# Kernel optimization log

Hardware: AMD Instinct MI355X
Metric: run time of the kernel (lower is better)

Reference implementation:

```python
import jax, jax.numpy as jnp
import numpy as np

D_MODEL = 2048
D_INNER = 4096
D_STATE = 16
DT_RANK = 128
D_CONV = 4
EPS = 1e-5


def setup_inputs() -> dict:
    key = jax.random.key(0)
    ks = jax.random.split(key, 10)
    b, l = 1, 1024
    s = 0.02
    x = jax.random.normal(ks[0], (b, l, D_MODEL), jnp.float32)
    w_norm = jnp.ones((D_MODEL,), jnp.float32)
    W_in = jax.random.normal(ks[1], (D_MODEL, 2 * D_INNER), jnp.float32) * s
    conv_w = jax.random.normal(ks[2], (D_CONV, D_INNER), jnp.float32) * 0.3
    conv_b = jnp.zeros((D_INNER,), jnp.float32)
    W_xp = jax.random.normal(ks[3], (D_INNER, DT_RANK + 2 * D_STATE), jnp.float32) * s
    W_dt = jax.random.normal(ks[4], (DT_RANK, D_INNER), jnp.float32) * s
    b_dt = jnp.full((D_INNER,), -4.0, jnp.float32)  # softplus(-4) ~ small dt
    A_log = jnp.log(jnp.tile(jnp.arange(1, D_STATE + 1, dtype=jnp.float32), (D_INNER, 1)))
    D = jnp.ones((D_INNER,), jnp.float32)
    W_out = jax.random.normal(ks[5], (D_INNER, D_MODEL), jnp.float32) * s
    return dict(x=x, w_norm=w_norm, W_in=W_in, conv_w=conv_w, conv_b=conv_b,
                W_xp=W_xp, W_dt=W_dt, b_dt=b_dt, A_log=A_log, D=D, W_out=W_out)


def _rmsnorm(x, w):
    return x * jax.lax.rsqrt(jnp.mean(jnp.square(x), axis=-1, keepdims=True) + EPS) * w


def _depthwise_causal_conv(x, conv_w, conv_b):
    # x: (b, l, d_inner), conv_w: (d_conv, d_inner)
    k = conv_w[:, None, :]  # (W, I/groups=1, O)
    y = jax.lax.conv_general_dilated(
        x, k, window_strides=(1,), padding=((D_CONV - 1, 0),),
        dimension_numbers=('NWC', 'WIO', 'NWC'), feature_group_count=D_INNER)
    return y + conv_b


def _selective_scan(u, delta, A, B, C, D):
    # u, delta: (b,l,d); A: (d,n); B,C: (b,l,n); D: (d,)
    deltaA = jnp.exp(jnp.einsum('bld,dn->bldn', delta, A))          # (b,l,d,n)
    deltaBu = jnp.einsum('bld,bln,bld->bldn', delta, B, u)          # (b,l,d,n)
    dA = jnp.moveaxis(deltaA, 1, 0)    # (l,b,d,n)
    dBu = jnp.moveaxis(deltaBu, 1, 0)  # (l,b,d,n)
    Ct = jnp.moveaxis(C, 1, 0)         # (l,b,n)
    b, l, d = u.shape
    n = A.shape[1]

    def step(h, inputs):
        dA_t, dBu_t, C_t = inputs
        h = h * dA_t + dBu_t                       # (b,d,n)
        y = jnp.einsum('bdn,bn->bd', h, C_t)       # (b,d)
        return h, y

    h0 = jnp.zeros((b, d, n), u.dtype)
    _, ys = jax.lax.scan(step, h0, (dA, dBu, Ct))
    y = jnp.moveaxis(ys, 0, 1)                     # (b,l,d)
    return y + u * D


def reference(x, w_norm, W_in, conv_w, conv_b, W_xp, W_dt, b_dt, A_log, D, W_out):
    # ResidualBlock: out = MambaBlock(RMSNorm(x)) + x
    xn = _rmsnorm(x, w_norm)
    xz = xn @ W_in                                  # (b,l,2*d_inner)
    xs, res = jnp.split(xz, 2, axis=-1)
    xs = _depthwise_causal_conv(xs, conv_w, conv_b)
    xs = jax.nn.silu(xs)
    # SSM
    A = -jnp.exp(A_log)                             # (d_inner, n)
    xdbc = xs @ W_xp                                # (b,l,dt_rank+2n)
    dt_r = xdbc[..., :DT_RANK]
    B = xdbc[..., DT_RANK:DT_RANK + D_STATE]
    C = xdbc[..., DT_RANK + D_STATE:]
    delta = jax.nn.softplus(dt_r @ W_dt + b_dt)     # (b,l,d_inner)
    y = _selective_scan(xs, delta, A, B, C, D)
    y = y * jax.nn.silu(res)
    out = y @ W_out + x
    return out
```

## Files before the change

kernel.cpp:

```cpp
#include <hip/hip_runtime.h>
#include <math.h>

#define L_SEQ   1024
#define DMODEL  2048
#define DINNER  4096
#define DSTATE  16
#define DTRANK  128
#define N_XZ    (2 * DINNER)
#define N_XP    (DTRANK + 2 * DSTATE)
#define EPS_F   1e-5f
#define NCHUNK  32
#define TCH     32
#define SK_XP   16

using bf16x8 = __attribute__((ext_vector_type(8))) short;
using f32x4  = __attribute__((ext_vector_type(4))) float;

__device__ __forceinline__ float silu_f(float v) {
    return v * (1.0f / (1.0f + __expf(-v)));
}
__device__ __forceinline__ float softplus_f(float v) {
    return (v > 15.0f) ? v : log1pf(__expf(v));
}
__device__ __forceinline__ unsigned short f2bf(float f) {
    unsigned b = __float_as_uint(f);
    return (unsigned short)((b + 0x7FFFu + ((b >> 16) & 1u)) >> 16);
}

#define GLOAD_LDS(gp, lp) \
    __builtin_amdgcn_global_load_lds((const __attribute__((address_space(1))) void*)(gp), \
                                     (__attribute__((address_space(3))) void*)(lp), 16, 0, 0)

__global__ __launch_bounds__(256) void transpose_bf16_kernel(const float* __restrict__ W,
                                                             unsigned short* __restrict__ BT,
                                                             int K, int N) {
    __shared__ unsigned short Tl[32][72];
    const int k0 = blockIdx.y * 64, n0 = blockIdx.x * 32;
    const int kr = threadIdx.x >> 3;
    const int nc = (threadIdx.x & 7) * 4;
    float4 v0 = *(const float4*)&W[(size_t)(k0 + kr) * N + n0 + nc];
    float4 v1 = *(const float4*)&W[(size_t)(k0 + kr + 32) * N + n0 + nc];
    Tl[nc + 0][kr] = f2bf(v0.x); Tl[nc + 1][kr] = f2bf(v0.y);
    Tl[nc + 2][kr] = f2bf(v0.z); Tl[nc + 3][kr] = f2bf(v0.w);
    Tl[nc + 0][kr + 32] = f2bf(v1.x); Tl[nc + 1][kr + 32] = f2bf(v1.y);
    Tl[nc + 2][kr + 32] = f2bf(v1.z); Tl[nc + 3][kr + 32] = f2bf(v1.w);
    __syncthreads();
    const int n = threadIdx.x >> 3;
    const int k8 = (threadIdx.x & 7) * 8;
    *(bf16x8*)&BT[(size_t)(n0 + n) * K + k0 + k8] = *(const bf16x8*)&Tl[n][k8];
}

__global__ __launch_bounds__(256) void rmsnorm_kernel(const float* __restrict__ x,
                                                      const float* __restrict__ w,
                                                      unsigned short* __restrict__ xn) {
    const int row = blockIdx.x;
    const float4* xr = (const float4*)(x + (size_t)row * DMODEL);
    float ss = 0.f;
    float4 v0 = xr[threadIdx.x];
    float4 v1 = xr[threadIdx.x + 256];
    ss += v0.x*v0.x + v0.y*v0.y + v0.z*v0.z + v0.w*v0.w;
    ss += v1.x*v1.x + v1.y*v1.y + v1.z*v1.z + v1.w*v1.w;
    #pragma unroll
    for (int o = 32; o > 0; o >>= 1) ss += __shfl_down(ss, o);
    __shared__ float red[4];
    const int lane = threadIdx.x & 63, wv = threadIdx.x >> 6;
    if (lane == 0) red[wv] = ss;
    __syncthreads();
    if (threadIdx.x == 0) {
        float t = red[0] + red[1] + red[2] + red[3];
        red[0] = rsqrtf(t / (float)DMODEL + EPS_F);
    }
    __syncthreads();
    const float scale = red[0];
    const float4* wr = (const float4*)w;
    float4 w0 = wr[threadIdx.x];
    float4 w1 = wr[threadIdx.x + 256];
    ushort4 o0, o1;
    o0.x = f2bf(v0.x * scale * w0.x); o0.y = f2bf(v0.y * scale * w0.y);
    o0.z = f2bf(v0.z * scale * w0.z); o0.w = f2bf(v0.w * scale * w0.w);
    o1.x = f2bf(v1.x * scale * w1.x); o1.y = f2bf(v1.y * scale * w1.y);
    o1.z = f2bf(v1.z * scale * w1.z); o1.w = f2bf(v1.w * scale * w1.w);
    unsigned short* outr = xn + (size_t)row * DMODEL;
    *(ushort4*)&outr[threadIdx.x * 4] = o0;
    *(ushort4*)&outr[1024 + threadIdx.x * 4] = o1;
}

template <int BM, int BN, int MODE>
__global__ __launch_bounds__(256) void gemm_mfma_kernel(const unsigned short* __restrict__ A,
                                                        const unsigned short* __restrict__ BT,
                                                        float* __restrict__ C,
                                                        int K, int Kc, int ldc, int Ncols,
                                                        const float* __restrict__ bias,
                                                        const float* __restrict__ resid) {
    constexpr int MT = BM / 32;
    constexpr int NT = BN / 32;
    __shared__ __align__(16) unsigned short Al[BM * 32];
    __shared__ __align__(16) unsigned short Bl[BN * 32];
    const int tid = threadIdx.x;
    const int lane = tid & 63, wave = tid >> 6;
    const int wm = wave >> 1, wn = wave & 1;
    const int bm = blockIdx.y * BM, bn = blockIdx.x * BN;
    const size_t koff = (size_t)blockIdx.z * Kc;
    C += (size_t)blockIdx.z * (size_t)gridDim.y * BM * ldc;
    const int sr = lane >> 2;
    const int sk = (((lane & 3) ^ ((sr >> 1) & 3))) * 8;
    const int fr = lane & 15;
    const int fq = lane >> 4;
    const int fsw = (fq ^ ((fr >> 1) & 3)) * 8;

    f32x4 acc[MT][NT];
    #pragma unroll
    for (int i = 0; i < MT; ++i)
        #pragma unroll
        for (int j = 0; j < NT; ++j)
            acc[i][j] = (f32x4){0.f, 0.f, 0.f, 0.f};

    for (int k0 = 0; k0 < Kc; k0 += 32) {
        #pragma unroll
        for (int is = wave; is < BM / 16; is += 4)
            GLOAD_LDS(&A[(size_t)(bm + is * 16 + sr) * K + koff + k0 + sk], &Al[is * 512]);
        #pragma unroll
        for (int is = wave; is < BN / 16; is += 4)
            GLOAD_LDS(&BT[(size_t)(bn + is * 16 + sr) * K + koff + k0 + sk], &Bl[is * 512]);
        __syncthreads();
        bf16x8 af[MT], bfr[NT];
        #pragma unroll
        for (int i = 0; i < MT; ++i)
            af[i] = *(const bf16x8*)&Al[(wm * (BM / 2) + i * 16 + fr) * 32 + fsw];
        #pragma unroll
        for (int j = 0; j < NT; ++j)
            bfr[j] = *(const bf16x8*)&Bl[(wn * (BN / 2) + j * 16 + fr) * 32 + fsw];
        #pragma unroll
        for (int i = 0; i < MT; ++i)
            #pragma unroll
            for (int j = 0; j < NT; ++j)
                acc[i][j] = __builtin_amdgcn_mfma_f32_16x16x32_bf16(af[i], bfr[j], acc[i][j], 0, 0, 0);
        __syncthreads();
    }

    #pragma unroll
    for (int i = 0; i < MT; ++i) {
        const int row = bm + wm * (BM / 2) + i * 16 + fq * 4;
        #pragma unroll
        for (int j = 0; j < NT; ++j) {
            const int col = bn + wn * (BN / 2) + j * 16 + fr;
            if (col < Ncols) {
                #pragma unroll
                for (int r = 0; r < 4; ++r) {
                    float v = acc[i][j][r];
                    if (MODE == 1) v = softplus_f(v + bias[col]);
                    if (MODE == 2) v += resid[(size_t)(row + r) * ldc + col];
                    C[(size_t)(row + r) * ldc + col] = v;
                }
            }
        }
    }
}

__global__ __launch_bounds__(256) void conv_silu_kernel(const float* __restrict__ xz,
                                                        const float* __restrict__ cw,
                                                        const float* __restrict__ cb,
                                                        float* __restrict__ xs,
                                                        unsigned short* __restrict__ xs_bf) {
    const int idx = blockIdx.x * 256 + threadIdx.x;
    const int t = idx >> 12;
    const int c = idx & (DINNER - 1);
    float acc = cb[c];
    #pragma unroll
    for (int k = 0; k < 4; ++k) {
        const int tt = t + k - 3;
        if (tt >= 0) acc = fmaf(xz[(size_t)tt * N_XZ + c], cw[k * DINNER + c], acc);
    }
    const float s = silu_f(acc);
    xs[idx] = s;
    xs_bf[idx] = f2bf(s);
}

__global__ __launch_bounds__(256) void reduce_sk_kernel(const float* __restrict__ part,
                                                        float* __restrict__ xdbc,
                                                        unsigned short* __restrict__ xdbc_dt) {
    const int i = blockIdx.x * 256 + threadIdx.x;
    float s = 0.f;
    #pragma unroll
    for (int c = 0; c < SK_XP; ++c) s += part[(size_t)c * (L_SEQ * N_XP) + i];
    xdbc[i] = s;
    const int col = i % N_XP;
    if (col < DTRANK) xdbc_dt[(i / N_XP) * DTRANK + col] = f2bf(s);
}

__global__ __launch_bounds__(256) void scan_pass1(const float* __restrict__ delta,
                                                  const float* __restrict__ xs,
                                                  const float* __restrict__ xdbc,
                                                  const float* __restrict__ A_log,
                                                  float* __restrict__ S,
                                                  float* __restrict__ sumdl) {
    __shared__ float BC[TCH][32];
    const int c = blockIdx.y;
    const int d = blockIdx.x * 256 + threadIdx.x;
    const int t0 = c * TCH;
    {
        const int tt = threadIdx.x >> 3, q = threadIdx.x & 7;
        *(float4*)&BC[tt][q * 4] =
            *(const float4*)&xdbc[(size_t)(t0 + tt) * N_XP + DTRANK + q * 4];
    }
    __syncthreads();
    float Aa[16];
    #pragma unroll
    for (int n = 0; n < 16; ++n) Aa[n] = -__expf(A_log[d * 16 + n]);
    float h[16];
    #pragma unroll
    for (int n = 0; n < 16; ++n) h[n] = 0.f;
    float sd = 0.f;
    for (int t = 0; t < TCH; ++t) {
        const float dl = delta[(size_t)(t0 + t) * DINNER + d];
        const float u  = xs[(size_t)(t0 + t) * DINNER + d];
        sd += dl;
        const float du = dl * u;
        #pragma unroll
        for (int n = 0; n < 16; ++n)
            h[n] = fmaf(h[n], __expf(dl * Aa[n]), du * BC[t][n]);
    }
    float* Sp = &S[((size_t)c * DINNER + d) * 16];
    #pragma unroll
    for (int n = 0; n < 16; n += 4)
        *(float4*)&Sp[n] = make_float4(h[n], h[n + 1], h[n + 2], h[n + 3]);
    sumdl[c * DINNER + d] = sd;
}

__global__ __launch_bounds__(256) void scan_pass2(const float* __restrict__ S,
                                                  const float* __restrict__ sumdl,
                                                  const float* __restrict__ A_log,
                                                  float* __restrict__ h0) {
    const int i = blockIdx.x * 256 + threadIdx.x;
    const int dd = i >> 4;
    const float A = -__expf(A_log[i]);
    float h = 0.f;
    #pragma unroll
    for (int c = 0; c < NCHUNK; ++c) {
        h0[(size_t)c * (DINNER * 16) + i] = h;
        h = h * __expf(A * sumdl[c * DINNER + dd]) + S[(size_t)c * (DINNER * 16) + i];
    }
}

__global__ __launch_bounds__(256) void scan_pass3(const float* __restrict__ delta,
                                                  const float* __restrict__ xs,
                                                  const float* __restrict__ xdbc,
                                                  const float* __restrict__ xz,
                                                  const float* __restrict__ A_log,
                                                  const float* __restrict__ Dp,
                                                  const float* __restrict__ h0,
                                                  unsigned short* __restrict__ yg_bf) {
    __shared__ float BC[TCH][32];
    const int c = blockIdx.y;
    const int d = blockIdx.x * 256 + threadIdx.x;
    const int t0 = c * TCH;
    {
        const int tt = threadIdx.x >> 3, q = threadIdx.x & 7;
        *(float4*)&BC[tt][q * 4] =
            *(const float4*)&xdbc[(size_t)(t0 + tt) * N_XP + DTRANK + q * 4];
    }
    __syncthreads();
    float Aa[16];
    #pragma unroll
    for (int n = 0; n < 16; ++n) Aa[n] = -__expf(A_log[d * 16 + n]);
    float h[16];
    const float* h0p = &h0[(size_t)c * (DINNER * 16) + d * 16];
    #pragma unroll
    for (int n = 0; n < 16; n += 4) {
        float4 v = *(const float4*)&h0p[n];
        h[n] = v.x; h[n + 1] = v.y; h[n + 2] = v.z; h[n + 3] = v.w;
    }
    const float Dd = Dp[d];
    for (int t = 0; t < TCH; ++t) {
        const float dl = delta[(size_t)(t0 + t) * DINNER + d];
        const float u  = xs[(size_t)(t0 + t) * DINNER + d];
        const float du = dl * u;
        float y = 0.f;
        #pragma unroll
        for (int n = 0; n < 16; ++n) {
            h[n] = fmaf(h[n], __expf(dl * Aa[n]), du * BC[t][n]);
            y = fmaf(h[n], BC[t][16 + n], y);
        }
        const float res = xz[(size_t)(t0 + t) * N_XZ + DINNER + d];
        yg_bf[(size_t)(t0 + t) * DINNER + d] = f2bf((y + u * Dd) * silu_f(res));
    }
}

extern "C" void kernel_launch(void* const* d_in, const int* in_sizes, int n_in,
                              void* d_out, int out_size, void* d_ws, size_t ws_size,
                              hipStream_t stream) {
    const float* x     = (const float*)d_in[0];
    const float* wn    = (const float*)d_in[1];
    const float* W_in  = (const float*)d_in[2];
    const float* cw    = (const float*)d_in[3];
    const float* cb    = (const float*)d_in[4];
    const float* W_xp  = (const float*)d_in[5];
    const float* W_dt  = (const float*)d_in[6];
    const float* b_dt  = (const float*)d_in[7];
    const float* A_log = (const float*)d_in[8];
    const float* Dp    = (const float*)d_in[9];
    const float* W_out = (const float*)d_in[10];
    float* out = (float*)d_out;

    float* ws = (float*)d_ws;
    float*          xz    = ws;
    float*          xs    = xz + 8388608;
    float*          delta = xs + 4194304;
    float*          xdbc  = delta + 4194304;
    float*          part  = xdbc + 163840;
    float*          S     = part;
    float*          sumdl = S + 2097152;
    float*          h0    = part + 2621440;
    unsigned short* xn_bf = (unsigned short*)(h0 + 2097152);
    unsigned short* BTxp  = xn_bf;
    unsigned short* BTdt  = BTxp + 655360;
    unsigned short* xdbc_dt = BTdt + 524288;
    unsigned short* xs_bf = xn_bf + 2097152;
    unsigned short* yg_bf = xs_bf + 4194304;
    unsigned short* BT    = yg_bf + 4194304;

    transpose_bf16_kernel<<<dim3(N_XZ / 32, DMODEL / 64), 256, 0, stream>>>(W_in, BT, DMODEL, N_XZ);
    rmsnorm_kernel<<<L_SEQ, 256, 0, stream>>>(x, wn, xn_bf);
    gemm_mfma_kernel<64, 128, 0><<<dim3(N_XZ / 128, L_SEQ / 64), 256, 0, stream>>>(
        xn_bf, BT, xz, DMODEL, DMODEL, N_XZ, N_XZ, nullptr, nullptr);
    conv_silu_kernel<<<(L_SEQ * DINNER) / 256, 256, 0, stream>>>(xz, cw, cb, xs, xs_bf);
    transpose_bf16_kernel<<<dim3(N_XP / 32, DINNER / 64), 256, 0, stream>>>(W_xp, BTxp, DINNER, N_XP);
    transpose_bf16_kernel<<<dim3(DINNER / 32, DTRANK / 64), 256, 0, stream>>>(W_dt, BTdt, DTRANK, DINNER);
    gemm_mfma_kernel<128, 64, 0><<<dim3(3, L_SEQ / 128, SK_XP), 256, 0, stream>>>(
        xs_bf, BTxp, part, DINNER, DINNER / SK_XP, N_XP, N_XP, nullptr, nullptr);
    reduce_sk_kernel<<<(L_SEQ * N_XP) / 256, 256, 0, stream>>>(part, xdbc, xdbc_dt);
    gemm_mfma_kernel<64, 64, 1><<<dim3(DINNER / 64, L_SEQ / 64), 256, 0, stream>>>(
        xdbc_dt, BTdt, delta, DTRANK, DTRANK, DINNER, DINNER, b_dt, nullptr);
    scan_pass1<<<dim3(DINNER / 256, NCHUNK), 256, 0, stream>>>(delta, xs, xdbc, A_log, S, sumdl);
    scan_pass2<<<(DINNER * 16) / 256, 256, 0, stream>>>(S, sumdl, A_log, h0);
    scan_pass3<<<dim3(DINNER / 256, NCHUNK), 256, 0, stream>>>(delta, xs, xdbc, xz, A_log, Dp, h0, yg_bf);
    transpose_bf16_kernel<<<dim3(DMODEL / 32, DINNER / 64), 256, 0, stream>>>(W_out, BT, DINNER, DMODEL);
    gemm_mfma_kernel<64, 64, 2><<<dim3(DMODEL / 64, L_SEQ / 64), 256, 0, stream>>>(
        yg_bf, BT, out, DINNER, DINNER, DMODEL, DMODEL, nullptr, x);
}
```

Measured before the change: 356.9 us.

## Store intermediates in bf16, merge prep kernels, split-K output GEMM

Merges all weight transposes and the RMSNorm into one prep kernel to cut launches. Stores xz, xs and delta as bf16 instead of fp32 to halve intermediate traffic in the conv and scan kernels, and drops the fp32 xs copy. The input GEMM now uses 128x128 tiles, and the output GEMM is split-K by two with a separate reduce kernel that adds the residual. The change lowers precision of intermediates, including the gate and delta, and adds an extra reduction pass.

```diff
diff --git a/kernel.cpp b/kernel.cpp
--- a/kernel.cpp
+++ b/kernel.cpp
@@ -12,6 +12,7 @@
 #define NCHUNK  32
 #define TCH     32
 #define SK_XP   16
+#define SK_OUT  2
 
 using bf16x8 = __attribute__((ext_vector_type(8))) short;
 using f32x4  = __attribute__((ext_vector_type(4))) float;
@@ -26,16 +27,19 @@
     unsigned b = __float_as_uint(f);
     return (unsigned short)((b + 0x7FFFu + ((b >> 16) & 1u)) >> 16);
 }
+__device__ __forceinline__ float bf2f(unsigned short u) {
+    return __uint_as_float((unsigned)u << 16);
+}
 
 #define GLOAD_LDS(gp, lp) \
     __builtin_amdgcn_global_load_lds((const __attribute__((address_space(1))) void*)(gp), \
                                      (__attribute__((address_space(3))) void*)(lp), 16, 0, 0)
 
-__global__ __launch_bounds__(256) void transpose_bf16_kernel(const float* __restrict__ W,
-                                                             unsigned short* __restrict__ BT,
-                                                             int K, int N) {
-    __shared__ unsigned short Tl[32][72];
-    const int k0 = blockIdx.y * 64, n0 = blockIdx.x * 32;
+__device__ __forceinline__ void transpose_body(const float* __restrict__ W,
+                                               unsigned short* __restrict__ BT,
+                                               int K, int N, int bx, int by,
+                                               unsigned short (*Tl)[72]) {
+    const int k0 = by * 64, n0 = bx * 32;
     const int kr = threadIdx.x >> 3;
     const int nc = (threadIdx.x & 7) * 4;
     float4 v0 = *(const float4*)&W[(size_t)(k0 + kr) * N + n0 + nc];
@@ -50,48 +54,70 @@
     *(bf16x8*)&BT[(size_t)(n0 + n) * K + k0 + k8] = *(const bf16x8*)&Tl[n][k8];
 }
 
-__global__ __launch_bounds__(256) void rmsnorm_kernel(const float* __restrict__ x,
-                                                      const float* __restrict__ w,
-                                                      unsigned short* __restrict__ xn) {
-    const int row = blockIdx.x;
-    const float4* xr = (const float4*)(x + (size_t)row * DMODEL);
-    float ss = 0.f;
-    float4 v0 = xr[threadIdx.x];
-    float4 v1 = xr[threadIdx.x + 256];
-    ss += v0.x*v0.x + v0.y*v0.y + v0.z*v0.z + v0.w*v0.w;
-    ss += v1.x*v1.x + v1.y*v1.y + v1.z*v1.z + v1.w*v1.w;
-    #pragma unroll
-    for (int o = 32; o > 0; o >>= 1) ss += __shfl_down(ss, o);
+__global__ __launch_bounds__(256) void prep_kernel(const float* __restrict__ W_in,
+                                                   const float* __restrict__ W_xp,
+                                                   const float* __restrict__ W_dt,
+                                                   const float* __restrict__ W_out,
+                                                   const float* __restrict__ x,
+                                                   const float* __restrict__ wn,
+                                                   unsigned short* __restrict__ BT_in,
+                                                   unsigned short* __restrict__ BTxp,
+                                                   unsigned short* __restrict__ BTdt,
+                                                   unsigned short* __restrict__ BT_out,
+                                                   unsigned short* __restrict__ xn_bf) {
+    __shared__ unsigned short Tl[32][72];
     __shared__ float red[4];
-    const int lane = threadIdx.x & 63, wv = threadIdx.x >> 6;
-    if (lane == 0) red[wv] = ss;
-    __syncthreads();
-    if (threadIdx.x == 0) {
-        float t = red[0] + red[1] + red[2] + red[3];
-        red[0] = rsqrtf(t / (float)DMODEL + EPS_F);
-    }
-    __syncthreads();
-    const float scale = red[0];
-    const float4* wr = (const float4*)w;
-    float4 w0 = wr[threadIdx.x];
-    float4 w1 = wr[threadIdx.x + 256];
-    ushort4 o0, o1;
-    o0.x = f2bf(v0.x * scale * w0.x); o0.y = f2bf(v0.y * scale * w0.y);
-    o0.z = f2bf(v0.z * scale * w0.z); o0.w = f2bf(v0.w * scale * w0.w);
-    o1.x = f2bf(v1.x * scale * w1.x); o1.y = f2bf(v1.y * scale * w1.y);
-    o1.z = f2bf(v1.z * scale * w1.z); o1.w = f2bf(v1.w * scale * w1.w);
-    unsigned short* outr = xn + (size_t)row * DMODEL;
-    *(ushort4*)&outr[threadIdx.x * 4] = o0;
-    *(ushort4*)&outr[1024 + threadIdx.x * 4] = o1;
-}
-
-template <int BM, int BN, int MODE>
+    int b = blockIdx.x;
+    if (b < 8192) {
+        transpose_body(W_in, BT_in, DMODEL, N_XZ, b % 256, b / 256, Tl);
+    } else if (b < 12288) {
+        b -= 8192;
+        transpose_body(W_out, BT_out, DINNER, DMODEL, b % 64, b / 64, Tl);
+    } else if (b < 12608) {
+        b -= 12288;
+        transpose_body(W_xp, BTxp, DINNER, N_XP, b % 5, b / 5, Tl);
+    } else if (b < 12864) {
+        b -= 12608;
+        transpose_body(W_dt, BTdt, DTRANK, DINNER, b % 128, b / 128, Tl);
+    } else {
+        const int row = b - 12864;
+        const float4* xr = (const float4*)(x + (size_t)row * DMODEL);
+        float ss = 0.f;
+        float4 v0 = xr[threadIdx.x];
+        float4 v1 = xr[threadIdx.x + 256];
+        ss += v0.x*v0.x + v0.y*v0.y + v0.z*v0.z + v0.w*v0.w;
+        ss += v1.x*v1.x + v1.y*v1.y + v1.z*v1.z + v1.w*v1.w;
+        #pragma unroll
+        for (int o = 32; o > 0; o >>= 1) ss += __shfl_down(ss, o);
+        const int lane = threadIdx.x & 63, wv = threadIdx.x >> 6;
+        if (lane == 0) red[wv] = ss;
+        __syncthreads();
+        if (threadIdx.x == 0) {
+            float t = red[0] + red[1] + red[2] + red[3];
+            red[0] = rsqrtf(t / (float)DMODEL + EPS_F);
+        }
+        __syncthreads();
+        const float scale = red[0];
+        const float4* wr = (const float4*)wn;
+        float4 w0 = wr[threadIdx.x];
+        float4 w1 = wr[threadIdx.x + 256];
+        ushort4 o0, o1;
+        o0.x = f2bf(v0.x * scale * w0.x); o0.y = f2bf(v0.y * scale * w0.y);
+        o0.z = f2bf(v0.z * scale * w0.z); o0.w = f2bf(v0.w * scale * w0.w);
+        o1.x = f2bf(v1.x * scale * w1.x); o1.y = f2bf(v1.y * scale * w1.y);
+        o1.z = f2bf(v1.z * scale * w1.z); o1.w = f2bf(v1.w * scale * w1.w);
+        unsigned short* outr = xn_bf + (size_t)row * DMODEL;
+        *(ushort4*)&outr[threadIdx.x * 4] = o0;
+        *(ushort4*)&outr[1024 + threadIdx.x * 4] = o1;
+    }
+}
+
+template <int BM, int BN, int OUTM>
 __global__ __launch_bounds__(256) void gemm_mfma_kernel(const unsigned short* __restrict__ A,
                                                         const unsigned short* __restrict__ BT,
-                                                        float* __restrict__ C,
+                                                        void* __restrict__ Cv,
                                                         int K, int Kc, int ldc, int Ncols,
-                                                        const float* __restrict__ bias,
-                                                        const float* __restrict__ resid) {
+                                                        const float* __restrict__ bias) {
     constexpr int MT = BM / 32;
     constexpr int NT = BN / 32;
     __shared__ __align__(16) unsigned short Al[BM * 32];
@@ -101,7 +127,7 @@
     const int wm = wave >> 1, wn = wave & 1;
     const int bm = blockIdx.y * BM, bn = blockIdx.x * BN;
     const size_t koff = (size_t)blockIdx.z * Kc;
-    C += (size_t)blockIdx.z * (size_t)gridDim.y * BM * ldc;
+    const size_t zCoff = (size_t)blockIdx.z * (size_t)gridDim.y * BM * ldc;
     const int sr = lane >> 2;
     const int sk = (((lane & 3) ^ ((sr >> 1) & 3))) * 8;
     const int fr = lane & 15;
@@ -148,19 +174,23 @@
                 #pragma unroll
                 for (int r = 0; r < 4; ++r) {
                     float v = acc[i][j][r];
-                    if (MODE == 1) v = softplus_f(v + bias[col]);
-                    if (MODE == 2) v += resid[(size_t)(row + r) * ldc + col];
-                    C[(size_t)(row + r) * ldc + col] = v;
+                    if (OUTM == 0) {
+                        ((unsigned short*)Cv)[(size_t)(row + r) * ldc + col] = f2bf(v);
+                    } else if (OUTM == 1) {
+                        ((unsigned short*)Cv)[(size_t)(row + r) * ldc + col] =
+                            f2bf(softplus_f(v + bias[col]));
+                    } else {
+                        ((float*)Cv + zCoff)[(size_t)(row + r) * ldc + col] = v;
+                    }
                 }
             }
         }
     }
 }
 
-__global__ __launch_bounds__(256) void conv_silu_kernel(const float* __restrict__ xz,
+__global__ __launch_bounds__(256) void conv_silu_kernel(const unsigned short* __restrict__ xz_bf,
                                                         const float* __restrict__ cw,
                                                         const float* __restrict__ cb,
-                                                        float* __restrict__ xs,
                                                         unsigned short* __restrict__ xs_bf) {
     const int idx = blockIdx.x * 256 + threadIdx.x;
     const int t = idx >> 12;
@@ -169,11 +199,9 @@
     #pragma unroll
     for (int k = 0; k < 4; ++k) {
         const int tt = t + k - 3;
-        if (tt >= 0) acc = fmaf(xz[(size_t)tt * N_XZ + c], cw[k * DINNER + c], acc);
-    }
-    const float s = silu_f(acc);
-    xs[idx] = s;
-    xs_bf[idx] = f2bf(s);
+        if (tt >= 0) acc = fmaf(bf2f(xz_bf[(size_t)tt * N_XZ + c]), cw[k * DINNER + c], acc);
+    }
+    xs_bf[idx] = f2bf(silu_f(acc));
 }
 
 __global__ __launch_bounds__(256) void reduce_sk_kernel(const float* __restrict__ part,
@@ -188,8 +216,21 @@
     if (col < DTRANK) xdbc_dt[(i / N_XP) * DTRANK + col] = f2bf(s);
 }
 
-__global__ __launch_bounds__(256) void scan_pass1(const float* __restrict__ delta,
-                                                  const float* __restrict__ xs,
+__global__ __launch_bounds__(256) void reduce_out_kernel(const float* __restrict__ part,
+                                                         const float* __restrict__ x,
+                                                         float* __restrict__ out) {
+    const int i = blockIdx.x * 256 + threadIdx.x;
+    float4 a = ((const float4*)part)[i];
+    float4 b = ((const float4*)(part + (size_t)L_SEQ * DMODEL))[i];
+    float4 r = ((const float4*)x)[i];
+    float4 o;
+    o.x = a.x + b.x + r.x; o.y = a.y + b.y + r.y;
+    o.z = a.z + b.z + r.z; o.w = a.w + b.w + r.w;
+    ((float4*)out)[i] = o;
+}
+
+__global__ __launch_bounds__(256) void scan_pass1(const unsigned short* __restrict__ delta_bf,
+                                                  const unsigned short* __restrict__ xs_bf,
                                                   const float* __restrict__ xdbc,
                                                   const float* __restrict__ A_log,
                                                   float* __restrict__ S,
@@ -212,8 +253,8 @@
     for (int n = 0; n < 16; ++n) h[n] = 0.f;
     float sd = 0.f;
     for (int t = 0; t < TCH; ++t) {
-        const float dl = delta[(size_t)(t0 + t) * DINNER + d];
-        const float u  = xs[(size_t)(t0 + t) * DINNER + d];
+        const float dl = bf2f(delta_bf[(size_t)(t0 + t) * DINNER + d]);
+        const float u  = bf2f(xs_bf[(size_t)(t0 + t) * DINNER + d]);
         sd += dl;
         const float du = dl * u;
         #pragma unroll
@@ -242,10 +283,10 @@
     }
 }
 
-__global__ __launch_bounds__(256) void scan_pass3(const float* __restrict__ delta,
-                                                  const float* __restrict__ xs,
+__global__ __launch_bounds__(256) void scan_pass3(const unsigned short* __restrict__ delta_bf,
+                                                  const unsigned short* __restrict__ xs_bf,
                                                   const float* __restrict__ xdbc,
-                                                  const float* __restrict__ xz,
+                                                  const unsigned short* __restrict__ xz_bf,
                                                   const float* __restrict__ A_log,
                                                   const float* __restrict__ Dp,
                                                   const float* __restrict__ h0,
@@ -272,8 +313,8 @@
     }
     const float Dd = Dp[d];
     for (int t = 0; t < TCH; ++t) {
-        const float dl = delta[(size_t)(t0 + t) * DINNER + d];
-        const float u  = xs[(size_t)(t0 + t) * DINNER + d];
+        const float dl = bf2f(delta_bf[(size_t)(t0 + t) * DINNER + d]);
+        const float u  = bf2f(xs_bf[(size_t)(t0 + t) * DINNER + d]);
         const float du = dl * u;
         float y = 0.f;
         #pragma unroll
@@ -281,7 +322,7 @@
             h[n] = fmaf(h[n], __expf(dl * Aa[n]), du * BC[t][n]);
             y = fmaf(h[n], BC[t][16 + n], y);
         }
-        const float res = xz[(size_t)(t0 + t) * N_XZ + DINNER + d];
+        const float res = bf2f(xz_bf[(size_t)(t0 + t) * N_XZ + DINNER + d]);
         yg_bf[(size_t)(t0 + t) * DINNER + d] = f2bf((y + u * Dd) * silu_f(res));
     }
 }
@@ -303,38 +344,38 @@
     float* out = (float*)d_out;
 
     float* ws = (float*)d_ws;
-    float*          xz    = ws;
-    float*          xs    = xz + 8388608;
-    float*          delta = xs + 4194304;
-    float*          xdbc  = delta + 4194304;
-    float*          part  = xdbc + 163840;
-    float*          S     = part;
-    float*          sumdl = S + 2097152;
-    float*          h0    = part + 2621440;
-    unsigned short* xn_bf = (unsigned short*)(h0 + 2097152);
-    unsigned short* BTxp  = xn_bf;
-    unsigned short* BTdt  = BTxp + 655360;
-    unsigned short* xdbc_dt = BTdt + 524288;
-    unsigned short* xs_bf = xn_bf + 2097152;
-    unsigned short* yg_bf = xs_bf + 4194304;
-    unsigned short* BT    = yg_bf + 4194304;
-
-    transpose_bf16_kernel<<<dim3(N_XZ / 32, DMODEL / 64), 256, 0, stream>>>(W_in, BT, DMODEL, N_XZ);
-    rmsnorm_kernel<<<L_SEQ, 256, 0, stream>>>(x, wn, xn_bf);
-    gemm_mfma_kernel<64, 128, 0><<<dim3(N_XZ / 128, L_SEQ / 64), 256, 0, stream>>>(
-        xn_bf, BT, xz, DMODEL, DMODEL, N_XZ, N_XZ, nullptr, nullptr);
-    conv_silu_kernel<<<(L_SEQ * DINNER) / 256, 256, 0, stream>>>(xz, cw, cb, xs, xs_bf);
-    transpose_bf16_kernel<<<dim3(N_XP / 32, DINNER / 64), 256, 0, stream>>>(W_xp, BTxp, DINNER, N_XP);
-    transpose_bf16_kernel<<<dim3(DINNER / 32, DTRANK / 64), 256, 0, stream>>>(W_dt, BTdt, DTRANK, DINNER);
-    gemm_mfma_kernel<128, 64, 0><<<dim3(3, L_SEQ / 128, SK_XP), 256, 0, stream>>>(
-        xs_bf, BTxp, part, DINNER, DINNER / SK_XP, N_XP, N_XP, nullptr, nullptr);
+    unsigned short* xz_bf    = (unsigned short*)ws;
+    unsigned short* xs_bf    = (unsigned short*)(ws + 4194304);
+    unsigned short* yg_bf    = (unsigned short*)(ws + 6291456);
+    unsigned short* delta_bf = (unsigned short*)(ws + 8388608);
+    float*          part     = ws + 10485760;
+    float*          S        = part;
+    float*          sumdl    = S + 2097152;
+    float*          h0       = ws + 13107200;
+    float*          xdbc     = ws + 15204352;
+    unsigned short* xn_bf    = (unsigned short*)(ws + 15368192);
+    unsigned short* BTxp     = (unsigned short*)(ws + 16416768);
+    unsigned short* BTdt     = (unsigned short*)(ws + 16744448);
+    unsigned short* xdbc_dt  = (unsigned short*)(ws + 17006592);
+    unsigned short* BT_in    = (unsigned short*)(ws + 17072128);
+    unsigned short* BT_out   = (unsigned short*)(ws + 25460736);
+    float*          part_out = ws + 8388608;
+
+    prep_kernel<<<13888, 256, 0, stream>>>(W_in, W_xp, W_dt, W_out, x, wn,
+                                           BT_in, BTxp, BTdt, BT_out, xn_bf);
+    gemm_mfma_kernel<128, 128, 0><<<dim3(N_XZ / 128, L_SEQ / 128), 256, 0, stream>>>(
+        xn_bf, BT_in, xz_bf, DMODEL, DMODEL, N_XZ, N_XZ, nullptr);
+    conv_silu_kernel<<<(L_SEQ * DINNER) / 256, 256, 0, stream>>>(xz_bf, cw, cb, xs_bf);
+    gemm_mfma_kernel<128, 64, 2><<<dim3(3, L_SEQ / 128, SK_XP), 256, 0, stream>>>(
+        xs_bf, BTxp, part, DINNER, DINNER / SK_XP, N_XP, N_XP, nullptr);
     reduce_sk_kernel<<<(L_SEQ * N_XP) / 256, 256, 0, stream>>>(part, xdbc, xdbc_dt);
     gemm_mfma_kernel<64, 64, 1><<<dim3(DINNER / 64, L_SEQ / 64), 256, 0, stream>>>(
-        xdbc_dt, BTdt, delta, DTRANK, DTRANK, DINNER, DINNER, b_dt, nullptr);
-    scan_pass1<<<dim3(DINNER / 256, NCHUNK), 256, 0, stream>>>(delta, xs, xdbc, A_log, S, sumdl);
+        xdbc_dt, BTdt, delta_bf, DTRANK, DTRANK, DINNER, DINNER, b_dt);
+    scan_pass1<<<dim3(DINNER / 256, NCHUNK), 256, 0, stream>>>(delta_bf, xs_bf, xdbc, A_log, S, sumdl);
     scan_pass2<<<(DINNER * 16) / 256, 256, 0, stream>>>(S, sumdl, A_log, h0);
-    scan_pass3<<<dim3(DINNER / 256, NCHUNK), 256, 0, stream>>>(delta, xs, xdbc, xz, A_log, Dp, h0, yg_bf);
-    transpose_bf16_kernel<<<dim3(DMODEL / 32, DINNER / 64), 256, 0, stream>>>(W_out, BT, DINNER, DMODEL);
-    gemm_mfma_kernel<64, 64, 2><<<dim3(DMODEL / 64, L_SEQ / 64), 256, 0, stream>>>(
-        yg_bf, BT, out, DINNER, DINNER, DMODEL, DMODEL, nullptr, x);
-}
+    scan_pass3<<<dim3(DINNER / 256, NCHUNK), 256, 0, stream>>>(delta_bf, xs_bf, xdbc, xz_bf,
+                                                               A_log, Dp, h0, yg_bf);
+    gemm_mfma_kernel<64, 64, 2><<<dim3(DMODEL / 64, L_SEQ / 64, SK_OUT), 256, 0, stream>>>(
+        yg_bf, BT_out, part_out, DINNER, DINNER / SK_OUT, DMODEL, DMODEL, nullptr);
+    reduce_out_kernel<<<(L_SEQ * DMODEL / 4) / 256, 256, 0, stream>>>(part_out, x, out);
+}
```

After: 340.0 us. 4.7% less time.
